# Performance work log

Measured on AMD Instinct MI355X. Metric: run time of the kernel, lower is better.

The kernel has to match this reference:

```python
import jax, jax.numpy as jnp
import numpy as np

B, C, D, H, W = 2, 64, 20, 20, 20
RATIO = 8
CQ = C // RATIO  # Q/K channels = 8


def setup_inputs() -> dict:
    key = jax.random.key(0)
    ks = jax.random.split(key, 8)
    s = 0.05
    return {
        "x": jax.random.normal(ks[0], (B, C, D, H, W), dtype=jnp.float32),
        "Wq": jax.random.normal(ks[1], (CQ, C), dtype=jnp.float32) * s,
        "bq": jax.random.normal(ks[2], (CQ,), dtype=jnp.float32) * s,
        "Wk": jax.random.normal(ks[3], (CQ, C), dtype=jnp.float32) * s,
        "bk": jax.random.normal(ks[4], (CQ,), dtype=jnp.float32) * s,
        "Wv": jax.random.normal(ks[5], (C, C), dtype=jnp.float32) * s,
        "bv": jax.random.normal(ks[6], (C,), dtype=jnp.float32) * s,
        "gamma": jax.random.normal(ks[7], (1,), dtype=jnp.float32) * s,
    }


def reference(x, Wq, bq, Wk, bk, Wv, bv, gamma):
    b, c, *spatial = x.shape
    n = int(np.prod(spatial))
    xf = x.reshape(b, c, n)  # [B, C, N]
    # 1x1 convs == per-position channel matmuls
    Q = jnp.einsum('oc,bcn->bon', Wq, xf) + bq[None, :, None]  # [B, Cq, N]
    K = jnp.einsum('oc,bcn->bon', Wk, xf) + bk[None, :, None]  # [B, Cq, N]
    V = jnp.einsum('oc,bcn->bon', Wv, xf) + bv[None, :, None]  # [B, C, N]
    # energy[b, n, m] = sum_q Q[b, q, n] * K[b, q, m]  (no scaling, as in source)
    energy = jnp.einsum('bqn,bqm->bnm', Q, K)  # [B, N, N]
    attention = jax.nn.softmax(energy, axis=-1)
    # out[b, c, n] = sum_m V[b, c, m] * attention[b, n, m]
    out = jnp.einsum('bcm,bnm->bcn', V, attention)
    out = out.reshape(b, c, *spatial)
    return gamma * out + x
```

## Files before the change

kernel.cpp:

```cpp
#include <hip/hip_runtime.h>
#include <hip/hip_bf16.h>

#define BB 2
#define CC 64
#define CQk 8
#define NN 8000
#define QT 4
#define NWAVE 8
#define NBLK32 250

using f32x4  = __attribute__((ext_vector_type(4))) float;
using bf16x8 = __attribute__((ext_vector_type(8))) short;
typedef unsigned short ushort_t;
typedef unsigned int uint_t;

__device__ __forceinline__ ushort_t f2bf(float f) {
    __hip_bfloat16 h = __float2bfloat16(f);
    return *reinterpret_cast<ushort_t*>(&h);
}

__device__ __forceinline__ float exp2_fast(float x) {
#if __has_builtin(__builtin_amdgcn_exp2f)
    return __builtin_amdgcn_exp2f(x);
#else
    return exp2f(x);
#endif
}

__device__ __forceinline__ uint_t pack_bf16(float a, float b) {
    const uint_t ua = __builtin_bit_cast(uint_t, a) + 0x8000u;
    const uint_t ub = __builtin_bit_cast(uint_t, b) + 0x8000u;
    return (ua >> 16) | (ub & 0xFFFF0000u);
}

__global__ void detect_dtype(const void* __restrict__ x, int* __restrict__ flag)
{
    const float* xf = (const float*)x;
    const int t = threadIdx.x;
    const float a = fabsf(xf[t * 8]);
    const int ok = (a > 9.765625e-4f && a < 16.0f) ? 1 : 0;
    const unsigned long long m = __ballot(ok);
    if (t == 0) flag[0] = (__popcll(m) >= 48) ? 1 : 0;
}

__device__ __forceinline__ float loadF(const void* p, size_t i, int isf) {
    return isf ? ((const float*)p)[i]
               : __bfloat162float(((const __hip_bfloat16*)p)[i]);
}

__global__ __launch_bounds__(640) void qkv_kernel(
    const void* __restrict__ x,
    const void* __restrict__ Wq, const void* __restrict__ bq,
    const void* __restrict__ Wk, const void* __restrict__ bk,
    const void* __restrict__ Wv, const void* __restrict__ bv,
    ushort_t* __restrict__ Qbf, ushort_t* __restrict__ Kfrag,
    ushort_t* __restrict__ Vfrag, const int* __restrict__ flag)
{
    __shared__ float sW[80][CC];
    __shared__ float sB[80];
    __shared__ float sX[CC][64];
    const int isf = flag[0];
    const int t = threadIdx.x;

    for (int i = t; i < 80 * CC; i += 640) {
        const int r = i >> 6, c = i & 63;
        float w;
        if (r < CQk)          w = loadF(Wq, (size_t)r * CC + c, isf);
        else if (r < 2 * CQk) w = loadF(Wk, (size_t)(r - CQk) * CC + c, isf);
        else                  w = loadF(Wv, (size_t)(r - 2 * CQk) * CC + c, isf);
        sW[r][c] = w;
    }
    if (t < 80) {
        float bias;
        if (t < CQk)          bias = loadF(bq, t, isf);
        else if (t < 2 * CQk) bias = loadF(bk, t - CQk, isf);
        else                  bias = loadF(bv, t - 2 * CQk, isf);
        sB[t] = bias;
    }
    const int blk = blockIdx.x;
    const int b = blk / 125;
    const int n0 = (blk % 125) * 64;
    for (int i = t; i < CC * 64; i += 640) {
        const int c = i >> 6, nl = i & 63;
        sX[c][nl] = loadF(x, (size_t)b * CC * NN + (size_t)c * NN + n0 + nl, isf);
    }
    __syncthreads();

    const int rg = t >> 6;
    const int nl = t & 63;
    const int n = n0 + nl;
    const int r0 = rg * 8;

    float xv[CC];
#pragma unroll
    for (int c = 0; c < CC; ++c) xv[c] = sX[c][nl];

    float acc[8];
#pragma unroll
    for (int rr = 0; rr < 8; ++rr) {
        const f32x4* w4 = (const f32x4*)&sW[r0 + rr][0];
        float a0 = 0.f, a1 = 0.f, a2 = 0.f, a3 = 0.f;
#pragma unroll
        for (int c4 = 0; c4 < 16; ++c4) {
            const f32x4 wv = w4[c4];
            a0 += wv.x * xv[c4 * 4 + 0];
            a1 += wv.y * xv[c4 * 4 + 1];
            a2 += wv.z * xv[c4 * 4 + 2];
            a3 += wv.w * xv[c4 * 4 + 3];
        }
        acc[rr] = sB[r0 + rr] + ((a0 + a1) + (a2 + a3));
    }

    const int mblk = n >> 5;
    if (rg == 0) {
        bf16x8 pq;
#pragma unroll
        for (int j = 0; j < 8; ++j) pq[j] = (short)f2bf(acc[j] * 1.44269504089f);
        *(bf16x8*)&Qbf[((size_t)b * NN + n) * 8] = pq;
    } else if (rg == 1) {
        bf16x8 pk, z8;
#pragma unroll
        for (int j = 0; j < 8; ++j) { pk[j] = (short)f2bf(acc[j]); z8[j] = 0; }
        const int rloc = n & 31, jj = rloc >> 4, cl16 = rloc & 15;
        ushort_t* kb = Kfrag + (size_t)b * NN * 32
                     + ((size_t)(mblk * 2 + jj) * 64) * 8;
        *(bf16x8*)&kb[(cl16) * 8]      = pk;
        *(bf16x8*)&kb[(16 + cl16) * 8] = z8;
        *(bf16x8*)&kb[(32 + cl16) * 8] = z8;
        *(bf16x8*)&kb[(48 + cl16) * 8] = z8;
    } else {
        const int c0 = (rg - 2) * 8;
        const int hv = (n & 15) >> 2;
        const int iv = (n & 3) + (((n >> 4) & 1) << 2);
        ushort_t* vb = Vfrag + (size_t)b * NN * 64;
#pragma unroll
        for (int rr = 0; rr < 8; ++rr) {
            const int c = c0 + rr;
            vb[((size_t)(mblk * 4 + (c >> 4)) * 64 + hv * 16 + (c & 15)) * 8 + iv]
                = f2bf(acc[rr]);
        }
    }
}

#define KSTEP (16 * 1024)
#define VSTEP (16 * 2048)

#define LOADK(d0, d1, ko) do { \
    d0 = *(const bf16x8*)(Kb + (ko)); \
    d1 = *(const bf16x8*)(Kb + (ko) + 512); } while (0)

#define LOADV(v0, v1, v2, v3, vo) do { \
    v0 = *(const bf16x8*)(Vb + (vo)); \
    v1 = *(const bf16x8*)(Vb + (vo) + 512); \
    v2 = *(const bf16x8*)(Vb + (vo) + 1024); \
    v3 = *(const bf16x8*)(Vb + (vo) + 1536); } while (0)

#define MKAF(af, eA, eB) do { \
    union { uint_t u[4]; bf16x8 v; } _u; \
    _u.u[0] = pack_bf16(exp2_fast(eA[0]), exp2_fast(eA[1])); \
    _u.u[1] = pack_bf16(exp2_fast(eA[2]), exp2_fast(eA[3])); \
    _u.u[2] = pack_bf16(exp2_fast(eB[0]), exp2_fast(eB[1])); \
    _u.u[3] = pack_bf16(exp2_fast(eB[2]), exp2_fast(eB[3])); \
    af = _u.v; } while (0)

#define COMPUTE(ka0, ka1, v0, v1, v2, v3) do { \
    f32x4 e00 = __builtin_amdgcn_mfma_f32_16x16x32_bf16(ka0, qb[0], zf, 0, 0, 0); \
    f32x4 e10 = __builtin_amdgcn_mfma_f32_16x16x32_bf16(ka1, qb[0], zf, 0, 0, 0); \
    f32x4 e01 = __builtin_amdgcn_mfma_f32_16x16x32_bf16(ka0, qb[1], zf, 0, 0, 0); \
    f32x4 e11 = __builtin_amdgcn_mfma_f32_16x16x32_bf16(ka1, qb[1], zf, 0, 0, 0); \
    f32x4 e02 = __builtin_amdgcn_mfma_f32_16x16x32_bf16(ka0, qb[2], zf, 0, 0, 0); \
    f32x4 e12 = __builtin_amdgcn_mfma_f32_16x16x32_bf16(ka1, qb[2], zf, 0, 0, 0); \
    f32x4 e03 = __builtin_amdgcn_mfma_f32_16x16x32_bf16(ka0, qb[3], zf, 0, 0, 0); \
    f32x4 e13 = __builtin_amdgcn_mfma_f32_16x16x32_bf16(ka1, qb[3], zf, 0, 0, 0); \
    bf16x8 af0, af1, af2, af3; \
    MKAF(af0, e00, e10); MKAF(af1, e01, e11); \
    MKAF(af2, e02, e12); MKAF(af3, e03, e13); \
    acc[0][0] = __builtin_amdgcn_mfma_f32_16x16x32_bf16(af0, v0, acc[0][0], 0, 0, 0); \
    acc[0][1] = __builtin_amdgcn_mfma_f32_16x16x32_bf16(af0, v1, acc[0][1], 0, 0, 0); \
    acc[0][2] = __builtin_amdgcn_mfma_f32_16x16x32_bf16(af0, v2, acc[0][2], 0, 0, 0); \
    acc[0][3] = __builtin_amdgcn_mfma_f32_16x16x32_bf16(af0, v3, acc[0][3], 0, 0, 0); \
    lac[0]    = __builtin_amdgcn_mfma_f32_16x16x32_bf16(af0, ones, lac[0], 0, 0, 0); \
    acc[1][0] = __builtin_amdgcn_mfma_f32_16x16x32_bf16(af1, v0, acc[1][0], 0, 0, 0); \
    acc[1][1] = __builtin_amdgcn_mfma_f32_16x16x32_bf16(af1, v1, acc[1][1], 0, 0, 0); \
    acc[1][2] = __builtin_amdgcn_mfma_f32_16x16x32_bf16(af1, v2, acc[1][2], 0, 0, 0); \
    acc[1][3] = __builtin_amdgcn_mfma_f32_16x16x32_bf16(af1, v3, acc[1][3], 0, 0, 0); \
    lac[1]    = __builtin_amdgcn_mfma_f32_16x16x32_bf16(af1, ones, lac[1], 0, 0, 0); \
    acc[2][0] = __builtin_amdgcn_mfma_f32_16x16x32_bf16(af2, v0, acc[2][0], 0, 0, 0); \
    acc[2][1] = __builtin_amdgcn_mfma_f32_16x16x32_bf16(af2, v1, acc[2][1], 0, 0, 0); \
    acc[2][2] = __builtin_amdgcn_mfma_f32_16x16x32_bf16(af2, v2, acc[2][2], 0, 0, 0); \
    acc[2][3] = __builtin_amdgcn_mfma_f32_16x16x32_bf16(af2, v3, acc[2][3], 0, 0, 0); \
    lac[2]    = __builtin_amdgcn_mfma_f32_16x16x32_bf16(af2, ones, lac[2], 0, 0, 0); \
    acc[3][0] = __builtin_amdgcn_mfma_f32_16x16x32_bf16(af3, v0, acc[3][0], 0, 0, 0); \
    acc[3][1] = __builtin_amdgcn_mfma_f32_16x16x32_bf16(af3, v1, acc[3][1], 0, 0, 0); \
    acc[3][2] = __builtin_amdgcn_mfma_f32_16x16x32_bf16(af3, v2, acc[3][2], 0, 0, 0); \
    acc[3][3] = __builtin_amdgcn_mfma_f32_16x16x32_bf16(af3, v3, acc[3][3], 0, 0, 0); \
    lac[3]    = __builtin_amdgcn_mfma_f32_16x16x32_bf16(af3, ones, lac[3], 0, 0, 0); \
} while (0)

__global__ __launch_bounds__(512, 2) void attn_fused(
    const ushort_t* __restrict__ Qbf, const ushort_t* __restrict__ Kfrag,
    const ushort_t* __restrict__ Vfrag,
    const void* __restrict__ x, const void* __restrict__ gamma,
    void* __restrict__ out, const int* __restrict__ flag)
{
    __shared__ float sO[64][65];
    __shared__ float sL[64];
    const int isf = flag[0];
    const int tid = threadIdx.x;
    const int lane = tid & 63;
    const int w = tid >> 6;
    const int cl = lane & 15, h = lane >> 4;
    const int q0 = blockIdx.x * 64;
    const int b = blockIdx.y;
    const size_t bN = (size_t)b * NN;

    for (int i = tid; i < 64 * 65; i += 512) (&sO[0][0])[i] = 0.f;
    if (tid < 64) sL[tid] = 0.f;
    __syncthreads();

    bf16x8 zero8;
#pragma unroll
    for (int j = 0; j < 8; ++j) zero8[j] = 0;
    bf16x8 qb[QT];
#pragma unroll
    for (int t = 0; t < QT; ++t) {
        bf16x8 z = zero8;
        if (h == 0) z = *(const bf16x8*)&Qbf[(bN + q0 + t * 16 + cl) * 8];
        qb[t] = z;
    }
    bf16x8 ones;
#pragma unroll
    for (int j = 0; j < 8; ++j) ones[j] = (short)0x3F80;

    const f32x4 zf = {0.f, 0.f, 0.f, 0.f};
    f32x4 acc[QT][4];
    f32x4 lac[QT];
#pragma unroll
    for (int t = 0; t < QT; ++t) {
        lac[t] = zf;
#pragma unroll
        for (int ct = 0; ct < 4; ++ct) acc[t][ct] = zf;
    }

    const ushort_t* Kb = Kfrag + bN * 32;
    const ushort_t* Vb = Vfrag + bN * 64;

    uint_t koA = (uint_t)w * 1024 + lane * 8;
    uint_t voA = (uint_t)w * 2048 + lane * 8;
    uint_t koB = koA + 8 * 1024;
    uint_t voB = voA + 8 * 2048;
    int baA = w, baB = w + 8;

    bf16x8 ka0A, ka1A, vA0, vA1, vA2, vA3;
    bf16x8 ka0B, ka1B, vB0, vB1, vB2, vB3;

    LOADK(ka0A, ka1A, koA); LOADV(vA0, vA1, vA2, vA3, voA);
    baA += 16; if (baA < NBLK32) { koA += KSTEP; voA += VSTEP; }

    const int cnt = (w < 2) ? 32 : 31;
    const int pairs = cnt >> 1;
    for (int p = 0; p < pairs; ++p) {
        LOADK(ka0B, ka1B, koB); LOADV(vB0, vB1, vB2, vB3, voB);
        baB += 16; if (baB < NBLK32) { koB += KSTEP; voB += VSTEP; }
        COMPUTE(ka0A, ka1A, vA0, vA1, vA2, vA3);
        LOADK(ka0A, ka1A, koA); LOADV(vA0, vA1, vA2, vA3, voA);
        baA += 16; if (baA < NBLK32) { koA += KSTEP; voA += VSTEP; }
        COMPUTE(ka0B, ka1B, vB0, vB1, vB2, vB3);
    }
    if (cnt & 1) COMPUTE(ka0A, ka1A, vA0, vA1, vA2, vA3);

#pragma unroll
    for (int t = 0; t < QT; ++t) {
#pragma unroll
        for (int ct = 0; ct < 4; ++ct)
#pragma unroll
            for (int r = 0; r < 4; ++r)
                atomicAdd(&sO[t * 16 + 4 * h + r][ct * 16 + cl], acc[t][ct][r]);
        if (cl == 0) {
#pragma unroll
            for (int r = 0; r < 4; ++r)
                atomicAdd(&sL[t * 16 + 4 * h + r], lac[t][r]);
        }
    }
    __syncthreads();

    const float g = loadF(gamma, 0, isf);
    const int qq = tid & 63;
    const int crow = tid >> 6;
    const float rL = 1.0f / sL[qq];
#pragma unroll
    for (int p = 0; p < 8; ++p) {
        const int c = p * 8 + crow;
        const size_t idx = ((size_t)b * CC + c) * NN + q0 + qq;
        if (isf) {
            const float xr = __builtin_nontemporal_load((const float*)x + idx);
            __builtin_nontemporal_store(g * sO[qq][c] * rL + xr, (float*)out + idx);
        } else {
            const float xr = __bfloat162float(((const __hip_bfloat16*)x)[idx]);
            ((__hip_bfloat16*)out)[idx] = __float2bfloat16(g * sO[qq][c] * rL + xr);
        }
    }
}

extern "C" void kernel_launch(void* const* d_in, const int* in_sizes, int n_in,
                              void* d_out, int out_size, void* d_ws, size_t ws_size,
                              hipStream_t stream)
{
    const void* x     = d_in[0];
    const void* Wq    = d_in[1];
    const void* bq    = d_in[2];
    const void* Wk    = d_in[3];
    const void* bk    = d_in[4];
    const void* Wv    = d_in[5];
    const void* bv    = d_in[6];
    const void* gamma = d_in[7];

    char* base = (char*)d_ws;
    int* flag = (int*)base;
    size_t off = 256;
    ushort_t* Qbf   = (ushort_t*)(base + off); off += (size_t)BB * NN * CQk * 2;
    ushort_t* Kfrag = (ushort_t*)(base + off); off += (size_t)BB * NN * 32 * 2;
    ushort_t* Vfrag = (ushort_t*)(base + off); off += (size_t)BB * NN * 64 * 2;

    detect_dtype<<<1, 64, 0, stream>>>(x, flag);

    qkv_kernel<<<dim3(250), 640, 0, stream>>>(x, Wq, bq, Wk, bk, Wv, bv,
                                              Qbf, Kfrag, Vfrag, flag);

    dim3 g2(NN / 64, BB);
    attn_fused<<<g2, 512, 0, stream>>>(Qbf, Kfrag, Vfrag, x, gamma, d_out, flag);
}
```

Before: 128.0 us.

## Stage K/V in shared memory for coalesced fragment writes; pin attention loop schedule

The QKV projection kernel now writes K and V results into shared-memory tiles and then repacks them into the MFMA fragment layouts with vectorized 16-byte stores. Before, each thread wrote scattered 2-byte stores for V and partial K rows. Separately, sched_barrier calls are placed around the load and compute phases of the attention main loop, so the compiler keeps the intended software-pipelined order of prefetch and MFMA work. The cost is an extra __syncthreads and more LDS use in the projection kernel, plus less freedom for the compiler to interleave instructions in the attention loop.

Measured after the change: 124.3 us. 2.9% less time.

```diff
diff --git a/kernel.cpp b/kernel.cpp
--- a/kernel.cpp
+++ b/kernel.cpp
@@ -59,6 +59,8 @@
     __shared__ float sW[80][CC];
     __shared__ float sB[80];
     __shared__ float sX[CC][64];
+    __shared__ float sV[CC][65];
+    __shared__ float sK[8][65];
     const int isf = flag[0];
     const int t = threadIdx.x;
 
@@ -79,65 +81,83 @@
     }
     const int blk = blockIdx.x;
     const int b = blk / 125;
-    const int n0 = (blk % 125) * 64;
+    const int n0loc = (blk % 125) * 64;
     for (int i = t; i < CC * 64; i += 640) {
         const int c = i >> 6, nl = i & 63;
-        sX[c][nl] = loadF(x, (size_t)b * CC * NN + (size_t)c * NN + n0 + nl, isf);
+        sX[c][nl] = loadF(x, (size_t)b * CC * NN + (size_t)c * NN + n0loc + nl, isf);
     }
     __syncthreads();
 
-    const int rg = t >> 6;
-    const int nl = t & 63;
-    const int n = n0 + nl;
-    const int r0 = rg * 8;
-
-    float xv[CC];
-#pragma unroll
-    for (int c = 0; c < CC; ++c) xv[c] = sX[c][nl];
-
-    float acc[8];
-#pragma unroll
-    for (int rr = 0; rr < 8; ++rr) {
-        const f32x4* w4 = (const f32x4*)&sW[r0 + rr][0];
-        float a0 = 0.f, a1 = 0.f, a2 = 0.f, a3 = 0.f;
-#pragma unroll
-        for (int c4 = 0; c4 < 16; ++c4) {
-            const f32x4 wv = w4[c4];
-            a0 += wv.x * xv[c4 * 4 + 0];
-            a1 += wv.y * xv[c4 * 4 + 1];
-            a2 += wv.z * xv[c4 * 4 + 2];
-            a3 += wv.w * xv[c4 * 4 + 3];
-        }
-        acc[rr] = sB[r0 + rr] + ((a0 + a1) + (a2 + a3));
-    }
-
-    const int mblk = n >> 5;
-    if (rg == 0) {
-        bf16x8 pq;
-#pragma unroll
-        for (int j = 0; j < 8; ++j) pq[j] = (short)f2bf(acc[j] * 1.44269504089f);
-        *(bf16x8*)&Qbf[((size_t)b * NN + n) * 8] = pq;
-    } else if (rg == 1) {
-        bf16x8 pk, z8;
-#pragma unroll
-        for (int j = 0; j < 8; ++j) { pk[j] = (short)f2bf(acc[j]); z8[j] = 0; }
-        const int rloc = n & 31, jj = rloc >> 4, cl16 = rloc & 15;
-        ushort_t* kb = Kfrag + (size_t)b * NN * 32
-                     + ((size_t)(mblk * 2 + jj) * 64) * 8;
-        *(bf16x8*)&kb[(cl16) * 8]      = pk;
-        *(bf16x8*)&kb[(16 + cl16) * 8] = z8;
-        *(bf16x8*)&kb[(32 + cl16) * 8] = z8;
-        *(bf16x8*)&kb[(48 + cl16) * 8] = z8;
+    {
+        const int rg = t >> 6;
+        const int nl = t & 63;
+        const int r0 = rg * 8;
+
+        float xv[CC];
+#pragma unroll
+        for (int c = 0; c < CC; ++c) xv[c] = sX[c][nl];
+
+        float acc[8];
+#pragma unroll
+        for (int rr = 0; rr < 8; ++rr) {
+            const f32x4* w4 = (const f32x4*)&sW[r0 + rr][0];
+            float a0 = 0.f, a1 = 0.f, a2 = 0.f, a3 = 0.f;
+#pragma unroll
+            for (int c4 = 0; c4 < 16; ++c4) {
+                const f32x4 wv = w4[c4];
+                a0 += wv.x * xv[c4 * 4 + 0];
+                a1 += wv.y * xv[c4 * 4 + 1];
+                a2 += wv.z * xv[c4 * 4 + 2];
+                a3 += wv.w * xv[c4 * 4 + 3];
+            }
+            acc[rr] = sB[r0 + rr] + ((a0 + a1) + (a2 + a3));
+        }
+
+        if (rg == 0) {
+            bf16x8 pq;
+#pragma unroll
+            for (int j = 0; j < 8; ++j) pq[j] = (short)f2bf(acc[j] * 1.44269504089f);
+            *(bf16x8*)&Qbf[((size_t)b * NN + n0loc + nl) * 8] = pq;
+        } else if (rg == 1) {
+#pragma unroll
+            for (int rr = 0; rr < 8; ++rr) sK[rr][nl] = acc[rr];
+        } else {
+            const int c0 = (rg - 2) * 8;
+#pragma unroll
+            for (int rr = 0; rr < 8; ++rr) sV[c0 + rr][nl] = acc[rr];
+        }
+    }
+    __syncthreads();
+
+    const int mblk0 = n0loc >> 5;
+    if (t < 512) {
+        const int mblk = t >> 8, ct = (t >> 6) & 3, lanep = t & 63;
+        const int hp = lanep >> 4, clp = lanep & 15;
+        const int c = ct * 16 + clp;
+        bf16x8 pv;
+#pragma unroll
+        for (int iv = 0; iv < 8; ++iv) {
+            const int nl = mblk * 32 + 4 * hp + (iv & 3) + ((iv >> 2) << 4);
+            pv[iv] = (short)f2bf(sV[c][nl]);
+        }
+        *(bf16x8*)&Vfrag[(size_t)b * NN * 64
+                         + ((size_t)((mblk0 + mblk) * 4 + ct) * 64 + lanep) * 8] = pv;
     } else {
-        const int c0 = (rg - 2) * 8;
-        const int hv = (n & 15) >> 2;
-        const int iv = (n & 3) + (((n >> 4) & 1) << 2);
-        ushort_t* vb = Vfrag + (size_t)b * NN * 64;
-#pragma unroll
-        for (int rr = 0; rr < 8; ++rr) {
-            const int c = c0 + rr;
-            vb[((size_t)(mblk * 4 + (c >> 4)) * 64 + hv * 16 + (c & 15)) * 8 + iv]
-                = f2bf(acc[rr]);
+#pragma unroll
+        for (int rep = 0; rep < 2; ++rep) {
+            const int f = (t - 512) + rep * 128;
+            const int mblk = f >> 7, j = (f >> 6) & 1, lanep = f & 63;
+            bf16x8 pk;
+            if (lanep < 16) {
+                const int nl = mblk * 32 + j * 16 + lanep;
+#pragma unroll
+                for (int kk = 0; kk < 8; ++kk) pk[kk] = (short)f2bf(sK[kk][nl]);
+            } else {
+#pragma unroll
+                for (int kk = 0; kk < 8; ++kk) pk[kk] = 0;
+            }
+            *(bf16x8*)&Kfrag[(size_t)b * NN * 32
+                             + ((size_t)((mblk0 + mblk) * 2 + j) * 64 + lanep) * 8] = pk;
         }
     }
 }
@@ -197,6 +217,8 @@
     lac[3]    = __builtin_amdgcn_mfma_f32_16x16x32_bf16(af3, ones, lac[3], 0, 0, 0); \
 } while (0)
 
+#define SBAR() __builtin_amdgcn_sched_barrier(0)
+
 __global__ __launch_bounds__(512, 2) void attn_fused(
     const ushort_t* __restrict__ Qbf, const ushort_t* __restrict__ Kfrag,
     const ushort_t* __restrict__ Vfrag,
@@ -256,16 +278,21 @@
 
     LOADK(ka0A, ka1A, koA); LOADV(vA0, vA1, vA2, vA3, voA);
     baA += 16; if (baA < NBLK32) { koA += KSTEP; voA += VSTEP; }
+    SBAR();
 
     const int cnt = (w < 2) ? 32 : 31;
     const int pairs = cnt >> 1;
     for (int p = 0; p < pairs; ++p) {
         LOADK(ka0B, ka1B, koB); LOADV(vB0, vB1, vB2, vB3, voB);
         baB += 16; if (baB < NBLK32) { koB += KSTEP; voB += VSTEP; }
+        SBAR();
         COMPUTE(ka0A, ka1A, vA0, vA1, vA2, vA3);
+        SBAR();
         LOADK(ka0A, ka1A, koA); LOADV(vA0, vA1, vA2, vA3, voA);
         baA += 16; if (baA < NBLK32) { koA += KSTEP; voA += VSTEP; }
+        SBAR();
         COMPUTE(ka0B, ka1B, vB0, vB1, vB2, vB3);
+        SBAR();
     }
     if (cnt & 1) COMPUTE(ka0A, ka1A, vA0, vA1, vA2, vA3);
 
```
